# Kernel tuning notes

Measured on AMD Instinct MI355X. Metric: run time of the kernel, lower is better.

## Reference

```python
import jax, jax.numpy as jnp
import numpy as np

# Lloyd-Max (Max 1960) optimal 16-level quantizer for N(0,1), bits=4
_CODEBOOK_4 = np.array([-2.7326, -2.069, -1.6181, -1.2562, -0.9424, -0.6568,
                        -0.3881, -0.1284, 0.1284, 0.3881, 0.6568, 0.9424,
                        1.2562, 1.6181, 2.069, 2.7326], dtype=np.float32)
DIM = 256


def setup_inputs() -> dict:
    key = jax.random.key(0)
    kx, kq = jax.random.split(key)
    x = jax.random.normal(kx, (4, 4096, DIM), dtype=jnp.float32)
    # orthogonal rotation via QR of a Gaussian matrix (mirrors torch.linalg.qr)
    rotation, _ = jnp.linalg.qr(jax.random.normal(kq, (DIM, DIM), dtype=jnp.float32))
    codebook = jnp.asarray(_CODEBOOK_4)
    return {"x": x, "rotation": rotation, "codebook": codebook}


def reference(x, rotation, codebook):
    shape = x.shape
    d = shape[-1]
    sqrt_d = jnp.sqrt(jnp.asarray(d, dtype=x.dtype))
    x_flat = x.reshape(-1, d)                                   # (N, d)
    x_norm = jnp.maximum(
        jnp.linalg.norm(x_flat, axis=-1, keepdims=True), 1e-8)  # (N, 1)
    u = x_flat / x_norm                                         # unit vectors
    y_scaled = (u @ rotation.T) * sqrt_d                        # ~N(0,1) coords
    # nearest codebook entry per scalar coordinate: (N, d, K) -> argmin over K
    idx = jnp.argmin(jnp.abs(y_scaled[..., None] - codebook), axis=-1)
    y_hat = codebook[idx] / sqrt_d                              # (N, d)
    x_hat = (y_hat @ rotation) * x_norm                         # de-rotate, rescale
    return x_hat.reshape(shape)
```

## Files before the change

### kernel.cpp

```cpp
#include <hip/hip_runtime.h>

typedef _Float16 f16;
typedef _Float16 f16x4 __attribute__((ext_vector_type(4)));
typedef _Float16 f16x8 __attribute__((ext_vector_type(8)));
typedef float f32x16 __attribute__((ext_vector_type(16)));
typedef float f32x4 __attribute__((ext_vector_type(4)));

#define APITCH 264
#define WREG 67584

__global__ __launch_bounds__(512) void prep_kernel(const float* __restrict__ R,
                                                   f16* __restrict__ ws) {
  __shared__ float Lrs[32][260];
  const int b = blockIdx.x;
  const int g = b >> 2, h = b & 3;
  const int t = threadIdx.x;
  f16* W1h = ws;
  f16* W1l = ws + WREG;
  f16* W2h = ws + 2 * WREG;

  #pragma unroll
  for (int it = 0; it < 4; ++it) {
    int c = it * 512 + t;
    int row = c >> 6, c4 = (c & 63) * 4;
    f32x4 v = *(const f32x4*)&R[(long)(32 * g + row) * 256 + c4];
    *(f32x4*)&Lrs[row][c4] = v;
  }
  __syncthreads();

  if (t < 256) {
    int f_loc = 4 * h + (t >> 6), l = t & 63;
    int k0 = 16 * f_loc + 8 * (l >> 5);
    const float* src = &Lrs[l & 31][k0];
    f16x8 hi, lo;
    #pragma unroll
    for (int j = 0; j < 8; ++j) {
      float v = src[j] * 256.0f;
      f16 hh = (f16)v;
      hi[j] = hh;
      lo[j] = (f16)(v - (float)hh);
    }
    long o = (long)(g * 16 + f_loc) * 512 + l * 8;
    *(f16x8*)(W1h + o) = hi;
    *(f16x8*)(W1l + o) = lo;
  } else {
    int u = t - 256;
    int gp = 2 * h + (u >> 7), e = (u >> 6) & 1, l = u & 63;
    int lr0 = 16 * e + 8 * (l >> 5);
    int col = 32 * gp + (l & 31);
    f16x8 hv;
    #pragma unroll
    for (int j = 0; j < 8; ++j) hv[j] = (f16)Lrs[lr0 + j][col];
    long o = (long)(gp * 16 + 2 * g + e) * 512 + l * 8;
    *(f16x8*)(W2h + o) = hv;
  }
}

__global__ __launch_bounds__(512, 4) void tq_main(
    const float* __restrict__ X, const float* __restrict__ CB,
    const f16* __restrict__ ws, float* __restrict__ OUT) {
  __shared__ f16 A1h[32][APITCH];
  __shared__ f16 A1l[32][APITCH];
  __shared__ f16 Qs[32][APITCH];
  __shared__ float s2s[32];

  const int tid = threadIdx.x;
  const int lane = tid & 63;
  const int wv = tid >> 6;
  const int lrow = lane & 31;
  const int kg = lane >> 5;
  const long row0 = (long)blockIdx.x * 32;

  const f16* W1h = ws;
  const f16* W1l = ws + WREG;
  const f16* W2h = ws + 2 * WREG;

  const int r = tid >> 4, q = tid & 15;
  const float* xp = X + (row0 + r) * 256 + q * 16;
  float xa[16];
  #pragma unroll
  for (int i = 0; i < 4; ++i) {
    f32x4 v = ((const f32x4*)xp)[i];
    xa[4 * i] = v.x; xa[4 * i + 1] = v.y; xa[4 * i + 2] = v.z; xa[4 * i + 3] = v.w;
  }

  const f16* W1hp = W1h + (long)(wv * 16) * 512 + lane * 8;
  const f16* W1lp = W1l + (long)(wv * 16) * 512 + lane * 8;
  f16x8 bh0 = *(const f16x8*)(W1hp);
  f16x8 bl0 = *(const f16x8*)(W1lp);
  f16x8 bh1 = *(const f16x8*)(W1hp + 512);
  f16x8 bl1 = *(const f16x8*)(W1lp + 512);
  f16x8 bh2 = *(const f16x8*)(W1hp + 1024);
  f16x8 bl2 = *(const f16x8*)(W1lp + 1024);
  f16x8 bh3 = *(const f16x8*)(W1hp + 1536);
  f16x8 bl3 = *(const f16x8*)(W1lp + 1536);

  float cbf[16];
  #pragma unroll
  for (int i = 0; i < 16; ++i) cbf[i] = CB[i];

  float ss = 0.f;
  #pragma unroll
  for (int i = 0; i < 16; ++i) ss += xa[i] * xa[i];
  ss += __shfl_xor(ss, 8, 16);
  ss += __shfl_xor(ss, 4, 16);
  ss += __shfl_xor(ss, 2, 16);
  ss += __shfl_xor(ss, 1, 16);
  float nrm = fmaxf(sqrtf(ss), 1e-8f);
  float s1f = 4096.0f / nrm;
  if (q == 0) s2s[r] = nrm * 0.0625f;

  #pragma unroll
  for (int c8 = 0; c8 < 2; ++c8) {
    f16x8 h, l;
    #pragma unroll
    for (int j = 0; j < 8; ++j) {
      float a = xa[c8 * 8 + j] * s1f;
      f16 hh = (f16)a;
      h[j] = hh;
      l[j] = (f16)(a - (float)hh);
    }
    *(f16x8*)&A1h[r][q * 16 + c8 * 8] = h;
    *(f16x8*)&A1l[r][q * 16 + c8 * 8] = l;
  }
  __syncthreads();

  f32x16 zv;
  #pragma unroll
  for (int i = 0; i < 16; ++i) zv[i] = 0.0f;
  f32x16 accH = zv, accL = zv;

#define MM1_STAGE(BH, BL, KS)                                                   \
  {                                                                             \
    const int k0 = (KS) * 16 + kg * 8;                                          \
    f16x8 ah = *(const f16x8*)&A1h[lrow][k0];                                   \
    f16x8 al = *(const f16x8*)&A1l[lrow][k0];                                   \
    accH = __builtin_amdgcn_mfma_f32_32x32x16_f16(ah, BH, accH, 0, 0, 0);       \
    accL = __builtin_amdgcn_mfma_f32_32x32x16_f16(al, BH, accL, 0, 0, 0);       \
    accH = __builtin_amdgcn_mfma_f32_32x32x16_f16(ah, BL, accH, 0, 0, 0);       \
    BH = *(const f16x8*)(W1hp + ((KS) + 4) * 512);                              \
    BL = *(const f16x8*)(W1lp + ((KS) + 4) * 512);                              \
  }

  #pragma unroll
  for (int ksb = 0; ksb < 16; ksb += 4) {
    MM1_STAGE(bh0, bl0, ksb)
    MM1_STAGE(bh1, bl1, ksb + 1)
    MM1_STAGE(bh2, bl2, ksb + 2)
    MM1_STAGE(bh3, bl3, ksb + 3)
  }
#undef MM1_STAGE

  const f16* W2p = W2h + (long)(wv * 16) * 512 + lane * 8;
  f16x8 c0 = *(const f16x8*)(W2p);
  f16x8 c1 = *(const f16x8*)(W2p + 512);
  f16x8 c2 = *(const f16x8*)(W2p + 1024);
  f16x8 c3 = *(const f16x8*)(W2p + 1536);

  float M[15];
  #pragma unroll
  for (int t = 0; t < 15; ++t) M[t] = 65536.0f * (0.5f * (cbf[t] + cbf[t + 1]));
  unsigned int cpk[8];
  #pragma unroll
  for (int i = 0; i < 8; ++i) {
    unsigned short lb = __builtin_bit_cast(unsigned short, (f16)cbf[2 * i]);
    unsigned short hb = __builtin_bit_cast(unsigned short, (f16)cbf[2 * i + 1]);
    cpk[i] = ((unsigned int)hb << 16) | (unsigned int)lb;
  }

  #pragma unroll
  for (int rr = 0; rr < 16; ++rr) {
    float y = accH[rr] + accL[rr];
    int row = 4 * kg + (rr & 3) + 8 * (rr >> 2);
    int kk = 32 * wv + lrow;
    bool b3 = y > M[7];
    float m2 = b3 ? M[11] : M[3];
    bool b2 = y > m2;
    float m1 = b3 ? (b2 ? M[13] : M[9]) : (b2 ? M[5] : M[1]);
    bool b1 = y > m1;
    float m0 = b1 ? (b3 ? (b2 ? M[14] : M[10]) : (b2 ? M[6] : M[2]))
                  : (b3 ? (b2 ? M[12] : M[8]) : (b2 ? M[4] : M[0]));
    bool b0 = y > m0;
    unsigned int pp = b3 ? (b2 ? (b1 ? cpk[7] : cpk[6]) : (b1 ? cpk[5] : cpk[4]))
                         : (b2 ? (b1 ? cpk[3] : cpk[2]) : (b1 ? cpk[1] : cpk[0]));
    unsigned short qb = (unsigned short)(b0 ? (pp >> 16) : (pp & 0xFFFFu));
    Qs[row][kk] = __builtin_bit_cast(f16, qb);
  }
  __syncthreads();

  f32x16 acc2a = zv, acc2b = zv;
  #pragma unroll
  for (int ks = 0; ks < 16; ks += 4) {
    {
      f16x8 qa = *(const f16x8*)&Qs[lrow][ks * 16 + kg * 8];
      acc2a = __builtin_amdgcn_mfma_f32_32x32x16_f16(qa, c0, acc2a, 0, 0, 0);
      c0 = *(const f16x8*)(W2p + (ks + 4) * 512);
    }
    {
      f16x8 qa = *(const f16x8*)&Qs[lrow][(ks + 1) * 16 + kg * 8];
      acc2b = __builtin_amdgcn_mfma_f32_32x32x16_f16(qa, c1, acc2b, 0, 0, 0);
      c1 = *(const f16x8*)(W2p + (ks + 5) * 512);
    }
    {
      f16x8 qa = *(const f16x8*)&Qs[lrow][(ks + 2) * 16 + kg * 8];
      acc2a = __builtin_amdgcn_mfma_f32_32x32x16_f16(qa, c2, acc2a, 0, 0, 0);
      c2 = *(const f16x8*)(W2p + (ks + 6) * 512);
    }
    {
      f16x8 qa = *(const f16x8*)&Qs[lrow][(ks + 3) * 16 + kg * 8];
      acc2b = __builtin_amdgcn_mfma_f32_32x32x16_f16(qa, c3, acc2b, 0, 0, 0);
      c3 = *(const f16x8*)(W2p + (ks + 7) * 512);
    }
  }

  #pragma unroll
  for (int rr = 0; rr < 16; ++rr) {
    int row = 4 * kg + (rr & 3) + 8 * (rr >> 2);
    int col = 32 * wv + lrow;
    OUT[(row0 + row) * 256 + col] = (acc2a[rr] + acc2b[rr]) * s2s[row];
  }
}

#define FB_APITCH 264
#define FB_B1PITCH 40
#define FB_B2PITCH 264

__global__ __launch_bounds__(256, 1) void tq_main_fb(
    const float* __restrict__ X, const float* __restrict__ R,
    const float* __restrict__ CB, float* __restrict__ OUT) {
  __shared__ f16 A1h[64][FB_APITCH];
  __shared__ f16 A1l[64][FB_APITCH];
  __shared__ f16 Qs[64][FB_APITCH];
  __shared__ f32x4 Braw[2624];
  __shared__ float pn[4][64];
  __shared__ float s1s[64];
  __shared__ float s2s[64];

  f16 (*B1h)[FB_B1PITCH] = (f16(*)[FB_B1PITCH])Braw;
  f16 (*B1l)[FB_B1PITCH] = (f16(*)[FB_B1PITCH])((char*)Braw + 20480);
  f16 (*B2h)[FB_B2PITCH] = (f16(*)[FB_B2PITCH])Braw;

  const int tid = threadIdx.x;
  const int lane = tid & 63;
  const int wv = tid >> 6;
  const int lrow = lane & 31;
  const int kg = lane >> 5;
  const long row0 = (long)blockIdx.x * 64;

  float cbf[16];
  #pragma unroll
  for (int i = 0; i < 16; ++i) cbf[i] = CB[i];
  float M[15];
  #pragma unroll
  for (int t = 0; t < 15; ++t) M[t] = 65536.0f * (0.5f * (cbf[t] + cbf[t + 1]));
  unsigned int cpk[8];
  #pragma unroll
  for (int i = 0; i < 8; ++i) {
    unsigned short lb = __builtin_bit_cast(unsigned short, (f16)cbf[2 * i]);
    unsigned short hb = __builtin_bit_cast(unsigned short, (f16)cbf[2 * i + 1]);
    cpk[i] = ((unsigned int)hb << 16) | (unsigned int)lb;
  }

  const int xrow = tid >> 2, xq = tid & 3;
  const float* xp = X + (row0 + xrow) * 256 + xq * 64;
  float xa[64];
  #pragma unroll
  for (int i = 0; i < 16; ++i) {
    f32x4 v = ((const f32x4*)xp)[i];
    xa[4 * i] = v.x; xa[4 * i + 1] = v.y; xa[4 * i + 2] = v.z; xa[4 * i + 3] = v.w;
  }
  float ss = 0.f;
  #pragma unroll
  for (int i = 0; i < 64; ++i) ss += xa[i] * xa[i];
  pn[xq][xrow] = ss;
  __syncthreads();
  if (tid < 64) {
    float s = pn[0][tid] + pn[1][tid] + pn[2][tid] + pn[3][tid];
    float nrm = fmaxf(sqrtf(s), 1e-8f);
    s1s[tid] = 4096.0f / nrm;
    s2s[tid] = nrm * 0.0625f;
  }
  __syncthreads();

  {
    float s1f = s1s[xrow];
    #pragma unroll
    for (int c8 = 0; c8 < 8; ++c8) {
      f16x8 h, l;
      #pragma unroll
      for (int j = 0; j < 8; ++j) {
        float a = xa[c8 * 8 + j] * s1f;
        f16 hh = (f16)a;
        h[j] = hh;
        l[j] = (f16)(a - (float)hh);
      }
      *(f16x8*)&A1h[xrow][xq * 64 + c8 * 8] = h;
      *(f16x8*)&A1l[xrow][xq * 64 + c8 * 8] = l;
    }
  }

  f32x4 pf[8];
  #pragma unroll
  for (int q = 0; q < 8; ++q) {
    int c = q * 256 + tid;
    pf[q] = *(const f32x4*)&R[(long)(c >> 3) * 256 + ((c & 7) * 4)];
  }

  f32x16 zv;
  #pragma unroll
  for (int i = 0; i < 16; ++i) zv[i] = 0.0f;
  f32x16 acc[2][2];
  acc[0][0] = zv; acc[0][1] = zv; acc[1][0] = zv; acc[1][1] = zv;

  for (int kp = 0; kp < 8; ++kp) {
    __syncthreads();
    #pragma unroll
    for (int q = 0; q < 8; ++q) {
      int c = q * 256 + tid;
      int n = c >> 3, k4 = (c & 7) * 4;
      f16x4 h, l;
      #pragma unroll
      for (int j = 0; j < 4; ++j) {
        float sv = pf[q][j] * 256.0f;
        f16 hh = (f16)sv;
        h[j] = hh;
        l[j] = (f16)(sv - (float)hh);
      }
      *(f16x4*)&B1h[n][k4] = h;
      *(f16x4*)&B1l[n][k4] = l;
    }
    __syncthreads();
    if (kp < 7) {
      #pragma unroll
      for (int q = 0; q < 8; ++q) {
        int c = q * 256 + tid;
        pf[q] = *(const f32x4*)&R[(long)(c >> 3) * 256 + (kp + 1) * 32 + ((c & 7) * 4)];
      }
    }
    #pragma unroll
    for (int ks = 0; ks < 2; ++ks) {
      const int k0 = kp * 32 + ks * 16 + kg * 8;
      const int lk = ks * 16 + kg * 8;
      f16x8 ah[2], al[2], bhf[2], blf[2];
      #pragma unroll
      for (int m = 0; m < 2; ++m) {
        ah[m] = *(const f16x8*)&A1h[32 * m + lrow][k0];
        al[m] = *(const f16x8*)&A1l[32 * m + lrow][k0];
      }
      #pragma unroll
      for (int n = 0; n < 2; ++n) {
        int col = 64 * wv + 32 * n + lrow;
        bhf[n] = *(const f16x8*)&B1h[col][lk];
        blf[n] = *(const f16x8*)&B1l[col][lk];
      }
      #pragma unroll
      for (int m = 0; m < 2; ++m)
        #pragma unroll
        for (int n = 0; n < 2; ++n) {
          acc[m][n] = __builtin_amdgcn_mfma_f32_32x32x16_f16(ah[m], bhf[n], acc[m][n], 0, 0, 0);
          acc[m][n] = __builtin_amdgcn_mfma_f32_32x32x16_f16(al[m], bhf[n], acc[m][n], 0, 0, 0);
          acc[m][n] = __builtin_amdgcn_mfma_f32_32x32x16_f16(ah[m], blf[n], acc[m][n], 0, 0, 0);
          acc[m][n] = __builtin_amdgcn_mfma_f32_32x32x16_f16(al[m], blf[n], acc[m][n], 0, 0, 0);
        }
    }
  }

  #pragma unroll
  for (int q = 0; q < 8; ++q) {
    int c = q * 256 + tid;
    pf[q] = *(const f32x4*)&R[(long)(c >> 6) * 256 + ((c & 63) * 4)];
  }

  #pragma unroll
  for (int m = 0; m < 2; ++m)
    #pragma unroll
    for (int n = 0; n < 2; ++n)
      #pragma unroll
      for (int rr = 0; rr < 16; ++rr) {
        float y = acc[m][n][rr];
        int row = 32 * m + 4 * kg + (rr & 3) + 8 * (rr >> 2);
        int kk = 64 * wv + 32 * n + lrow;
        bool b3 = y > M[7];
        float m2 = b3 ? M[11] : M[3];
        bool b2 = y > m2;
        float m1 = b3 ? (b2 ? M[13] : M[9]) : (b2 ? M[5] : M[1]);
        bool b1 = y > m1;
        float m0 = b1 ? (b3 ? (b2 ? M[14] : M[10]) : (b2 ? M[6] : M[2]))
                      : (b3 ? (b2 ? M[12] : M[8]) : (b2 ? M[4] : M[0]));
        bool b0 = y > m0;
        unsigned int pp = b3 ? (b2 ? (b1 ? cpk[7] : cpk[6]) : (b1 ? cpk[5] : cpk[4]))
                             : (b2 ? (b1 ? cpk[3] : cpk[2]) : (b1 ? cpk[1] : cpk[0]));
        unsigned short qb = (unsigned short)(b0 ? (pp >> 16) : (pp & 0xFFFFu));
        Qs[row][kk] = __builtin_bit_cast(f16, qb);
      }
  __syncthreads();

  f32x16 acc2[2][2];
  acc2[0][0] = zv; acc2[0][1] = zv; acc2[1][0] = zv; acc2[1][1] = zv;

  for (int kp = 0; kp < 8; ++kp) {
    if (kp) __syncthreads();
    #pragma unroll
    for (int q = 0; q < 8; ++q) {
      int c = q * 256 + tid;
      int k = c >> 6, n4 = (c & 63) * 4;
      f16x4 h;
      #pragma unroll
      for (int j = 0; j < 4; ++j) h[j] = (f16)pf[q][j];
      *(f16x4*)&B2h[k][n4] = h;
    }
    __syncthreads();
    if (kp < 7) {
      #pragma unroll
      for (int q = 0; q < 8; ++q) {
        int c = q * 256 + tid;
        pf[q] = *(const f32x4*)&R[(long)((kp + 1) * 32 + (c >> 6)) * 256 + ((c & 63) * 4)];
      }
    }
    #pragma unroll
    for (int ks = 0; ks < 2; ++ks) {
      const int k0 = kp * 32 + ks * 16 + kg * 8;
      const int lk = ks * 16 + kg * 8;
      f16x8 qa[2], bb[2];
      #pragma unroll
      for (int m = 0; m < 2; ++m) qa[m] = *(const f16x8*)&Qs[32 * m + lrow][k0];
      #pragma unroll
      for (int n = 0; n < 2; ++n) {
        int colg = 64 * wv + 32 * n + lrow;
        #pragma unroll
        for (int j = 0; j < 8; ++j) bb[n][j] = B2h[lk + j][colg];
      }
      #pragma unroll
      for (int m = 0; m < 2; ++m)
        #pragma unroll
        for (int n = 0; n < 2; ++n)
          acc2[m][n] = __builtin_amdgcn_mfma_f32_32x32x16_f16(qa[m], bb[n], acc2[m][n], 0, 0, 0);
    }
  }

  #pragma unroll
  for (int m = 0; m < 2; ++m)
    #pragma unroll
    for (int n = 0; n < 2; ++n)
      #pragma unroll
      for (int rr = 0; rr < 16; ++rr) {
        int row = 32 * m + 4 * kg + (rr & 3) + 8 * (rr >> 2);
        int col = 64 * wv + 32 * n + lrow;
        OUT[(row0 + row) * 256 + col] = acc2[m][n][rr] * s2s[row];
      }
}

extern "C" void kernel_launch(void* const* d_in, const int* in_sizes, int n_in,
                              void* d_out, int out_size, void* d_ws, size_t ws_size,
                              hipStream_t stream) {
  const float* X = (const float*)d_in[0];
  const float* R = (const float*)d_in[1];
  const float* CB = (const float*)d_in[2];
  float* OUT = (float*)d_out;
  const int nrows = in_sizes[0] / 256;

  if (ws_size >= (size_t)3 * WREG * sizeof(f16)) {
    f16* ws = (f16*)d_ws;
    prep_kernel<<<32, 512, 0, stream>>>(R, ws);
    tq_main<<<nrows / 32, 512, 0, stream>>>(X, CB, ws, OUT);
  } else {
    tq_main_fb<<<nrows / 64, 256, 0, stream>>>(X, R, CB, OUT);
  }
}
```

Before: 25.40 us.

## Switch main kernel to 16-row tiles with 16x16x32 MFMA and repacked weights

Halves the rows per block from 32 to 16 and switches both matmuls from 32x32x16 to 16x16x32 MFMA instructions. Each wave now owns two 16-column output groups. The prep kernel repacks the rotation weights into the matching fragment layout, and the workspace offsets shrink to exact sizes. This doubles the grid to 1024 blocks and cuts LDS per block so more blocks fit per CU (launch bounds raised to 6), aiming at better occupancy and latency hiding. The cost is that each block rereads the full weight set from global memory/L2 for half as many rows, doubling weight traffic.

```diff
diff --git a/kernel.cpp b/kernel.cpp
--- a/kernel.cpp
+++ b/kernel.cpp
@@ -1,37 +1,39 @@
 #include <hip/hip_runtime.h>
 
 typedef _Float16 f16;
+typedef _Float16 f16x8 __attribute__((ext_vector_type(8)));
 typedef _Float16 f16x4 __attribute__((ext_vector_type(4)));
-typedef _Float16 f16x8 __attribute__((ext_vector_type(8)));
+typedef float f32x4 __attribute__((ext_vector_type(4)));
 typedef float f32x16 __attribute__((ext_vector_type(16)));
-typedef float f32x4 __attribute__((ext_vector_type(4)));
 
 #define APITCH 264
-#define WREG 67584
 
 __global__ __launch_bounds__(512) void prep_kernel(const float* __restrict__ R,
                                                    f16* __restrict__ ws) {
   __shared__ float Lrs[32][260];
   const int b = blockIdx.x;
-  const int g = b >> 2, h = b & 3;
+  const int g2 = b >> 2, h = b & 3;
   const int t = threadIdx.x;
   f16* W1h = ws;
-  f16* W1l = ws + WREG;
-  f16* W2h = ws + 2 * WREG;
+  f16* W1l = ws + 65536;
+  f16* W2h = ws + 131072;
 
   #pragma unroll
   for (int it = 0; it < 4; ++it) {
     int c = it * 512 + t;
     int row = c >> 6, c4 = (c & 63) * 4;
-    f32x4 v = *(const f32x4*)&R[(long)(32 * g + row) * 256 + c4];
+    f32x4 v = *(const f32x4*)&R[(long)(32 * g2 + row) * 256 + c4];
     *(f32x4*)&Lrs[row][c4] = v;
   }
   __syncthreads();
 
   if (t < 256) {
-    int f_loc = 4 * h + (t >> 6), l = t & 63;
-    int k0 = 16 * f_loc + 8 * (l >> 5);
-    const float* src = &Lrs[l & 31][k0];
+    int fi = t >> 6;
+    int gi = fi >> 1, ksi = fi & 1;
+    int l = t & 63;
+    int g = 2 * g2 + gi;
+    int ks = 2 * h + ksi;
+    const float* src = &Lrs[16 * gi + (l & 15)][32 * ks + 8 * (l >> 4)];
     f16x8 hi, lo;
     #pragma unroll
     for (int j = 0; j < 8; ++j) {
@@ -40,60 +42,63 @@
       hi[j] = hh;
       lo[j] = (f16)(v - (float)hh);
     }
-    long o = (long)(g * 16 + f_loc) * 512 + l * 8;
+    long o = (long)(g * 8 + ks) * 512 + l * 8;
     *(f16x8*)(W1h + o) = hi;
     *(f16x8*)(W1l + o) = lo;
   } else {
     int u = t - 256;
-    int gp = 2 * h + (u >> 7), e = (u >> 6) & 1, l = u & 63;
-    int lr0 = 16 * e + 8 * (l >> 5);
-    int col = 32 * gp + (l & 31);
+    int gp = 4 * h + (u >> 6);
+    int l = u & 63;
     f16x8 hv;
     #pragma unroll
-    for (int j = 0; j < 8; ++j) hv[j] = (f16)Lrs[lr0 + j][col];
-    long o = (long)(gp * 16 + 2 * g + e) * 512 + l * 8;
+    for (int j = 0; j < 8; ++j) hv[j] = (f16)Lrs[8 * (l >> 4) + j][16 * gp + (l & 15)];
+    long o = (long)(gp * 8 + g2) * 512 + l * 8;
     *(f16x8*)(W2h + o) = hv;
   }
 }
 
-__global__ __launch_bounds__(512, 4) void tq_main(
+__global__ __launch_bounds__(512, 6) void tq_main(
     const float* __restrict__ X, const float* __restrict__ CB,
     const f16* __restrict__ ws, float* __restrict__ OUT) {
-  __shared__ f16 A1h[32][APITCH];
-  __shared__ f16 A1l[32][APITCH];
-  __shared__ f16 Qs[32][APITCH];
-  __shared__ float s2s[32];
+  __shared__ f16 A1h[16][APITCH];
+  __shared__ f16 A1l[16][APITCH];
+  __shared__ f16 Qs[16][APITCH];
+  __shared__ float s2s[16];
 
   const int tid = threadIdx.x;
   const int lane = tid & 63;
   const int wv = tid >> 6;
-  const int lrow = lane & 31;
-  const int kg = lane >> 5;
-  const long row0 = (long)blockIdx.x * 32;
+  const int lcol = lane & 15;
+  const int kq = lane >> 4;
+  const long row0 = (long)blockIdx.x * 16;
 
   const f16* W1h = ws;
-  const f16* W1l = ws + WREG;
-  const f16* W2h = ws + 2 * WREG;
-
-  const int r = tid >> 4, q = tid & 15;
-  const float* xp = X + (row0 + r) * 256 + q * 16;
-  float xa[16];
-  #pragma unroll
-  for (int i = 0; i < 4; ++i) {
-    f32x4 v = ((const f32x4*)xp)[i];
-    xa[4 * i] = v.x; xa[4 * i + 1] = v.y; xa[4 * i + 2] = v.z; xa[4 * i + 3] = v.w;
-  }
-
-  const f16* W1hp = W1h + (long)(wv * 16) * 512 + lane * 8;
-  const f16* W1lp = W1l + (long)(wv * 16) * 512 + lane * 8;
-  f16x8 bh0 = *(const f16x8*)(W1hp);
-  f16x8 bl0 = *(const f16x8*)(W1lp);
-  f16x8 bh1 = *(const f16x8*)(W1hp + 512);
-  f16x8 bl1 = *(const f16x8*)(W1lp + 512);
-  f16x8 bh2 = *(const f16x8*)(W1hp + 1024);
-  f16x8 bl2 = *(const f16x8*)(W1lp + 1024);
-  f16x8 bh3 = *(const f16x8*)(W1hp + 1536);
-  f16x8 bl3 = *(const f16x8*)(W1lp + 1536);
+  const f16* W1l = ws + 65536;
+  const f16* W2h = ws + 131072;
+  const int g0 = 2 * wv, g1 = 2 * wv + 1;
+
+  const int r = tid >> 5, q = tid & 31;
+  const float* xp = X + (row0 + r) * 256 + q * 8;
+  float xa[8];
+  {
+    f32x4 v0 = ((const f32x4*)xp)[0];
+    f32x4 v1 = ((const f32x4*)xp)[1];
+    xa[0] = v0.x; xa[1] = v0.y; xa[2] = v0.z; xa[3] = v0.w;
+    xa[4] = v1.x; xa[5] = v1.y; xa[6] = v1.z; xa[7] = v1.w;
+  }
+
+  const f16* W1p0  = W1h + (long)(g0 * 8) * 512 + lane * 8;
+  const f16* W1lp0 = W1l + (long)(g0 * 8) * 512 + lane * 8;
+  const f16* W1p1  = W1h + (long)(g1 * 8) * 512 + lane * 8;
+  const f16* W1lp1 = W1l + (long)(g1 * 8) * 512 + lane * 8;
+  f16x8 h00 = *(const f16x8*)(W1p0);
+  f16x8 l00 = *(const f16x8*)(W1lp0);
+  f16x8 h10 = *(const f16x8*)(W1p1);
+  f16x8 l10 = *(const f16x8*)(W1lp1);
+  f16x8 h01 = *(const f16x8*)(W1p0 + 512);
+  f16x8 l01 = *(const f16x8*)(W1lp0 + 512);
+  f16x8 h11 = *(const f16x8*)(W1p1 + 512);
+  f16x8 l11 = *(const f16x8*)(W1lp1 + 512);
 
   float cbf[16];
   #pragma unroll
@@ -101,61 +106,63 @@
 
   float ss = 0.f;
   #pragma unroll
-  for (int i = 0; i < 16; ++i) ss += xa[i] * xa[i];
-  ss += __shfl_xor(ss, 8, 16);
-  ss += __shfl_xor(ss, 4, 16);
-  ss += __shfl_xor(ss, 2, 16);
-  ss += __shfl_xor(ss, 1, 16);
+  for (int i = 0; i < 8; ++i) ss += xa[i] * xa[i];
+  ss += __shfl_xor(ss, 16, 32);
+  ss += __shfl_xor(ss, 8, 32);
+  ss += __shfl_xor(ss, 4, 32);
+  ss += __shfl_xor(ss, 2, 32);
+  ss += __shfl_xor(ss, 1, 32);
   float nrm = fmaxf(sqrtf(ss), 1e-8f);
   float s1f = 4096.0f / nrm;
   if (q == 0) s2s[r] = nrm * 0.0625f;
 
-  #pragma unroll
-  for (int c8 = 0; c8 < 2; ++c8) {
+  {
     f16x8 h, l;
     #pragma unroll
     for (int j = 0; j < 8; ++j) {
-      float a = xa[c8 * 8 + j] * s1f;
+      float a = xa[j] * s1f;
       f16 hh = (f16)a;
       h[j] = hh;
       l[j] = (f16)(a - (float)hh);
     }
-    *(f16x8*)&A1h[r][q * 16 + c8 * 8] = h;
-    *(f16x8*)&A1l[r][q * 16 + c8 * 8] = l;
-  }
-  __syncthreads();
-
-  f32x16 zv;
-  #pragma unroll
-  for (int i = 0; i < 16; ++i) zv[i] = 0.0f;
-  f32x16 accH = zv, accL = zv;
-
-#define MM1_STAGE(BH, BL, KS)                                                   \
-  {                                                                             \
-    const int k0 = (KS) * 16 + kg * 8;                                          \
-    f16x8 ah = *(const f16x8*)&A1h[lrow][k0];                                   \
-    f16x8 al = *(const f16x8*)&A1l[lrow][k0];                                   \
-    accH = __builtin_amdgcn_mfma_f32_32x32x16_f16(ah, BH, accH, 0, 0, 0);       \
-    accL = __builtin_amdgcn_mfma_f32_32x32x16_f16(al, BH, accL, 0, 0, 0);       \
-    accH = __builtin_amdgcn_mfma_f32_32x32x16_f16(ah, BL, accH, 0, 0, 0);       \
-    BH = *(const f16x8*)(W1hp + ((KS) + 4) * 512);                              \
-    BL = *(const f16x8*)(W1lp + ((KS) + 4) * 512);                              \
-  }
-
-  #pragma unroll
-  for (int ksb = 0; ksb < 16; ksb += 4) {
-    MM1_STAGE(bh0, bl0, ksb)
-    MM1_STAGE(bh1, bl1, ksb + 1)
-    MM1_STAGE(bh2, bl2, ksb + 2)
-    MM1_STAGE(bh3, bl3, ksb + 3)
+    *(f16x8*)&A1h[r][q * 8] = h;
+    *(f16x8*)&A1l[r][q * 8] = l;
+  }
+  __syncthreads();
+
+  f32x4 zv4 = {0.f, 0.f, 0.f, 0.f};
+  f32x4 accH0 = zv4, accH1 = zv4, accL0 = zv4, accL1 = zv4;
+
+#define MM1_STAGE(BH0, BL0, BH1, BL1, KS)                                      \
+  {                                                                            \
+    const int koff = (KS) * 32 + kq * 8;                                       \
+    f16x8 ah = *(const f16x8*)&A1h[lcol][koff];                                \
+    f16x8 al = *(const f16x8*)&A1l[lcol][koff];                                \
+    accH0 = __builtin_amdgcn_mfma_f32_16x16x32_f16(ah, BH0, accH0, 0, 0, 0);   \
+    accH1 = __builtin_amdgcn_mfma_f32_16x16x32_f16(ah, BH1, accH1, 0, 0, 0);   \
+    accL0 = __builtin_amdgcn_mfma_f32_16x16x32_f16(al, BH0, accL0, 0, 0, 0);   \
+    accL1 = __builtin_amdgcn_mfma_f32_16x16x32_f16(al, BH1, accL1, 0, 0, 0);   \
+    accH0 = __builtin_amdgcn_mfma_f32_16x16x32_f16(ah, BL0, accH0, 0, 0, 0);   \
+    accH1 = __builtin_amdgcn_mfma_f32_16x16x32_f16(ah, BL1, accH1, 0, 0, 0);   \
+    BH0 = *(const f16x8*)(W1p0 + (((KS) + 2) & 7) * 512);                      \
+    BL0 = *(const f16x8*)(W1lp0 + (((KS) + 2) & 7) * 512);                     \
+    BH1 = *(const f16x8*)(W1p1 + (((KS) + 2) & 7) * 512);                      \
+    BL1 = *(const f16x8*)(W1lp1 + (((KS) + 2) & 7) * 512);                     \
+  }
+
+  #pragma unroll
+  for (int ksb = 0; ksb < 8; ksb += 2) {
+    MM1_STAGE(h00, l00, h10, l10, ksb)
+    MM1_STAGE(h01, l01, h11, l11, ksb + 1)
   }
 #undef MM1_STAGE
 
-  const f16* W2p = W2h + (long)(wv * 16) * 512 + lane * 8;
-  f16x8 c0 = *(const f16x8*)(W2p);
-  f16x8 c1 = *(const f16x8*)(W2p + 512);
-  f16x8 c2 = *(const f16x8*)(W2p + 1024);
-  f16x8 c3 = *(const f16x8*)(W2p + 1536);
+  const f16* W2p0 = W2h + (long)(g0 * 8) * 512 + lane * 8;
+  const f16* W2p1 = W2h + (long)(g1 * 8) * 512 + lane * 8;
+  f16x8 c00 = *(const f16x8*)(W2p0);
+  f16x8 c10 = *(const f16x8*)(W2p1);
+  f16x8 c01 = *(const f16x8*)(W2p0 + 512);
+  f16x8 c11 = *(const f16x8*)(W2p1 + 512);
 
   float M[15];
   #pragma unroll
@@ -168,56 +175,56 @@
     cpk[i] = ((unsigned int)hb << 16) | (unsigned int)lb;
   }
 
-  #pragma unroll
-  for (int rr = 0; rr < 16; ++rr) {
-    float y = accH[rr] + accL[rr];
-    int row = 4 * kg + (rr & 3) + 8 * (rr >> 2);
-    int kk = 32 * wv + lrow;
-    bool b3 = y > M[7];
-    float m2 = b3 ? M[11] : M[3];
-    bool b2 = y > m2;
-    float m1 = b3 ? (b2 ? M[13] : M[9]) : (b2 ? M[5] : M[1]);
-    bool b1 = y > m1;
-    float m0 = b1 ? (b3 ? (b2 ? M[14] : M[10]) : (b2 ? M[6] : M[2]))
-                  : (b3 ? (b2 ? M[12] : M[8]) : (b2 ? M[4] : M[0]));
-    bool b0 = y > m0;
-    unsigned int pp = b3 ? (b2 ? (b1 ? cpk[7] : cpk[6]) : (b1 ? cpk[5] : cpk[4]))
-                         : (b2 ? (b1 ? cpk[3] : cpk[2]) : (b1 ? cpk[1] : cpk[0]));
-    unsigned short qb = (unsigned short)(b0 ? (pp >> 16) : (pp & 0xFFFFu));
-    Qs[row][kk] = __builtin_bit_cast(f16, qb);
-  }
-  __syncthreads();
-
-  f32x16 acc2a = zv, acc2b = zv;
-  #pragma unroll
-  for (int ks = 0; ks < 16; ks += 4) {
-    {
-      f16x8 qa = *(const f16x8*)&Qs[lrow][ks * 16 + kg * 8];
-      acc2a = __builtin_amdgcn_mfma_f32_32x32x16_f16(qa, c0, acc2a, 0, 0, 0);
-      c0 = *(const f16x8*)(W2p + (ks + 4) * 512);
-    }
-    {
-      f16x8 qa = *(const f16x8*)&Qs[lrow][(ks + 1) * 16 + kg * 8];
-      acc2b = __builtin_amdgcn_mfma_f32_32x32x16_f16(qa, c1, acc2b, 0, 0, 0);
-      c1 = *(const f16x8*)(W2p + (ks + 5) * 512);
-    }
-    {
-      f16x8 qa = *(const f16x8*)&Qs[lrow][(ks + 2) * 16 + kg * 8];
-      acc2a = __builtin_amdgcn_mfma_f32_32x32x16_f16(qa, c2, acc2a, 0, 0, 0);
-      c2 = *(const f16x8*)(W2p + (ks + 6) * 512);
-    }
-    {
-      f16x8 qa = *(const f16x8*)&Qs[lrow][(ks + 3) * 16 + kg * 8];
-      acc2b = __builtin_amdgcn_mfma_f32_32x32x16_f16(qa, c3, acc2b, 0, 0, 0);
-      c3 = *(const f16x8*)(W2p + (ks + 7) * 512);
-    }
-  }
-
-  #pragma unroll
-  for (int rr = 0; rr < 16; ++rr) {
-    int row = 4 * kg + (rr & 3) + 8 * (rr >> 2);
-    int col = 32 * wv + lrow;
-    OUT[(row0 + row) * 256 + col] = (acc2a[rr] + acc2b[rr]) * s2s[row];
+#define QUANT(AH, AL, G)                                                       \
+  _Pragma("unroll")                                                            \
+  for (int rr = 0; rr < 4; ++rr) {                                             \
+    float y = AH[rr] + AL[rr];                                                 \
+    int row = kq * 4 + rr;                                                     \
+    int kk = 16 * (G) + lcol;                                                  \
+    bool b3 = y > M[7];                                                        \
+    float m2 = b3 ? M[11] : M[3];                                              \
+    bool b2 = y > m2;                                                          \
+    float m1 = b3 ? (b2 ? M[13] : M[9]) : (b2 ? M[5] : M[1]);                  \
+    bool b1 = y > m1;                                                          \
+    float m0 = b1 ? (b3 ? (b2 ? M[14] : M[10]) : (b2 ? M[6] : M[2]))           \
+                  : (b3 ? (b2 ? M[12] : M[8]) : (b2 ? M[4] : M[0]));           \
+    bool b0 = y > m0;                                                          \
+    unsigned int pp = b3 ? (b2 ? (b1 ? cpk[7] : cpk[6]) : (b1 ? cpk[5] : cpk[4])) \
+                         : (b2 ? (b1 ? cpk[3] : cpk[2]) : (b1 ? cpk[1] : cpk[0])); \
+    unsigned short qb = (unsigned short)(b0 ? (pp >> 16) : (pp & 0xFFFFu));    \
+    Qs[row][kk] = __builtin_bit_cast(f16, qb);                                 \
+  }
+
+  QUANT(accH0, accL0, g0)
+  QUANT(accH1, accL1, g1)
+#undef QUANT
+  __syncthreads();
+
+  f32x4 acc20 = zv4, acc21 = zv4;
+
+#define MM2_STAGE(C0, C1, KS)                                                  \
+  {                                                                            \
+    const int koff = (KS) * 32 + kq * 8;                                       \
+    f16x8 qa = *(const f16x8*)&Qs[lcol][koff];                                 \
+    acc20 = __builtin_amdgcn_mfma_f32_16x16x32_f16(qa, C0, acc20, 0, 0, 0);    \
+    acc21 = __builtin_amdgcn_mfma_f32_16x16x32_f16(qa, C1, acc21, 0, 0, 0);    \
+    C0 = *(const f16x8*)(W2p0 + (((KS) + 2) & 7) * 512);                       \
+    C1 = *(const f16x8*)(W2p1 + (((KS) + 2) & 7) * 512);                       \
+  }
+
+  #pragma unroll
+  for (int ksb = 0; ksb < 8; ksb += 2) {
+    MM2_STAGE(c00, c10, ksb)
+    MM2_STAGE(c01, c11, ksb + 1)
+  }
+#undef MM2_STAGE
+
+  #pragma unroll
+  for (int rr = 0; rr < 4; ++rr) {
+    int row = kq * 4 + rr;
+    float s2 = s2s[row];
+    OUT[(row0 + row) * 256 + 16 * g0 + lcol] = acc20[rr] * s2;
+    OUT[(row0 + row) * 256 + 16 * g1 + lcol] = acc21[rr] * s2;
   }
 }
 
@@ -459,10 +466,10 @@
   float* OUT = (float*)d_out;
   const int nrows = in_sizes[0] / 256;
 
-  if (ws_size >= (size_t)3 * WREG * sizeof(f16)) {
+  if (ws_size >= (size_t)3 * 65536 * sizeof(f16)) {
     f16* ws = (f16*)d_ws;
     prep_kernel<<<32, 512, 0, stream>>>(R, ws);
-    tq_main<<<nrows / 32, 512, 0, stream>>>(X, CB, ws, OUT);
+    tq_main<<<nrows / 16, 512, 0, stream>>>(X, CB, ws, OUT);
   } else {
     tq_main_fb<<<nrows / 64, 256, 0, stream>>>(X, R, CB, OUT);
   }
```

Measured after the change: 37.58 us. 48.0% more time.

## Merge MFMA accumulators, alias Qs onto A1h, raise occupancy to six blocks

Applied to the files above, without the earlier changes.

The split hi/lo accumulators in both matmuls are merged into single accumulators, which frees VGPRs. The quantized tile Qs now reuses the A1h shared buffer after an added barrier, which cuts LDS per block. Launch bounds go from 4 to 6 blocks per CU, and the codebook values are made wave-uniform with readfirstlane so they can sit in scalar registers. The aim is higher occupancy to hide latency, at the cost of serialising dependent MFMA chains on one accumulator and adding an extra barrier.

```diff
diff --git a/kernel.cpp b/kernel.cpp
--- a/kernel.cpp
+++ b/kernel.cpp
@@ -56,12 +56,16 @@
   }
 }
 
-__global__ __launch_bounds__(512, 4) void tq_main(
+__device__ __forceinline__ float rfl(float x) {
+  return __builtin_bit_cast(float,
+      __builtin_amdgcn_readfirstlane(__builtin_bit_cast(int, x)));
+}
+
+__global__ __launch_bounds__(512, 6) void tq_main(
     const float* __restrict__ X, const float* __restrict__ CB,
     const f16* __restrict__ ws, float* __restrict__ OUT) {
   __shared__ f16 A1h[32][APITCH];
   __shared__ f16 A1l[32][APITCH];
-  __shared__ f16 Qs[32][APITCH];
   __shared__ float s2s[32];
 
   const int tid = threadIdx.x;
@@ -97,7 +101,7 @@
 
   float cbf[16];
   #pragma unroll
-  for (int i = 0; i < 16; ++i) cbf[i] = CB[i];
+  for (int i = 0; i < 16; ++i) cbf[i] = rfl(CB[i]);
 
   float ss = 0.f;
   #pragma unroll
@@ -128,16 +132,16 @@
   f32x16 zv;
   #pragma unroll
   for (int i = 0; i < 16; ++i) zv[i] = 0.0f;
-  f32x16 accH = zv, accL = zv;
+  f32x16 acc = zv;
 
 #define MM1_STAGE(BH, BL, KS)                                                   \
   {                                                                             \
     const int k0 = (KS) * 16 + kg * 8;                                          \
     f16x8 ah = *(const f16x8*)&A1h[lrow][k0];                                   \
     f16x8 al = *(const f16x8*)&A1l[lrow][k0];                                   \
-    accH = __builtin_amdgcn_mfma_f32_32x32x16_f16(ah, BH, accH, 0, 0, 0);       \
-    accL = __builtin_amdgcn_mfma_f32_32x32x16_f16(al, BH, accL, 0, 0, 0);       \
-    accH = __builtin_amdgcn_mfma_f32_32x32x16_f16(ah, BL, accH, 0, 0, 0);       \
+    acc = __builtin_amdgcn_mfma_f32_32x32x16_f16(ah, BH, acc, 0, 0, 0);         \
+    acc = __builtin_amdgcn_mfma_f32_32x32x16_f16(al, BH, acc, 0, 0, 0);         \
+    acc = __builtin_amdgcn_mfma_f32_32x32x16_f16(ah, BL, acc, 0, 0, 0);         \
     BH = *(const f16x8*)(W1hp + ((KS) + 4) * 512);                              \
     BL = *(const f16x8*)(W1lp + ((KS) + 4) * 512);                              \
   }
@@ -168,9 +172,12 @@
     cpk[i] = ((unsigned int)hb << 16) | (unsigned int)lb;
   }
 
+  __syncthreads();
+
+  f16 (*Qs)[APITCH] = A1h;
   #pragma unroll
   for (int rr = 0; rr < 16; ++rr) {
-    float y = accH[rr] + accL[rr];
+    float y = acc[rr];
     int row = 4 * kg + (rr & 3) + 8 * (rr >> 2);
     int kk = 32 * wv + lrow;
     bool b3 = y > M[7];
@@ -188,27 +195,27 @@
   }
   __syncthreads();
 
-  f32x16 acc2a = zv, acc2b = zv;
+  f32x16 acc2 = zv;
   #pragma unroll
   for (int ks = 0; ks < 16; ks += 4) {
     {
       f16x8 qa = *(const f16x8*)&Qs[lrow][ks * 16 + kg * 8];
-      acc2a = __builtin_amdgcn_mfma_f32_32x32x16_f16(qa, c0, acc2a, 0, 0, 0);
+      acc2 = __builtin_amdgcn_mfma_f32_32x32x16_f16(qa, c0, acc2, 0, 0, 0);
       c0 = *(const f16x8*)(W2p + (ks + 4) * 512);
     }
     {
       f16x8 qa = *(const f16x8*)&Qs[lrow][(ks + 1) * 16 + kg * 8];
-      acc2b = __builtin_amdgcn_mfma_f32_32x32x16_f16(qa, c1, acc2b, 0, 0, 0);
+      acc2 = __builtin_amdgcn_mfma_f32_32x32x16_f16(qa, c1, acc2, 0, 0, 0);
       c1 = *(const f16x8*)(W2p + (ks + 5) * 512);
     }
     {
       f16x8 qa = *(const f16x8*)&Qs[lrow][(ks + 2) * 16 + kg * 8];
-      acc2a = __builtin_amdgcn_mfma_f32_32x32x16_f16(qa, c2, acc2a, 0, 0, 0);
+      acc2 = __builtin_amdgcn_mfma_f32_32x32x16_f16(qa, c2, acc2, 0, 0, 0);
       c2 = *(const f16x8*)(W2p + (ks + 6) * 512);
     }
     {
       f16x8 qa = *(const f16x8*)&Qs[lrow][(ks + 3) * 16 + kg * 8];
-      acc2b = __builtin_amdgcn_mfma_f32_32x32x16_f16(qa, c3, acc2b, 0, 0, 0);
+      acc2 = __builtin_amdgcn_mfma_f32_32x32x16_f16(qa, c3, acc2, 0, 0, 0);
       c3 = *(const f16x8*)(W2p + (ks + 7) * 512);
     }
   }
@@ -217,7 +224,7 @@
   for (int rr = 0; rr < 16; ++rr) {
     int row = 4 * kg + (rr & 3) + 8 * (rr >> 2);
     int col = 32 * wv + lrow;
-    OUT[(row0 + row) * 256 + col] = (acc2a[rr] + acc2b[rr]) * s2s[row];
+    OUT[(row0 + row) * 256 + col] = acc2[rr] * s2s[row];
   }
 }
 
```

Result: no change. 25.91 us (+2.0%).
